# Performance work log

Measured on AMD Instinct MI355X. Metric: run time of the kernel, lower is better.

Reference implementation:

```python
import jax, jax.numpy as jnp
import numpy as np

# GE2E batch structure: N_SPK speakers, M_UTT utterances each (grouped contiguously),
# first half enrollment (-> centroid), second half test.
N_SPK, M_UTT, D = 1024, 32, 512
M_ENR = M_UTT // 2
EPS = 1e-8  # F.cosine_similarity default eps (clamps norms)


def setup_inputs() -> dict:
    key = jax.random.key(0)
    emb = jax.random.normal(key, (N_SPK * M_UTT, D), dtype=jnp.float32)
    labels = jnp.repeat(jnp.arange(N_SPK, dtype=jnp.int64), M_UTT)
    alpha = jnp.asarray(10.0, dtype=jnp.float32)
    beta = jnp.asarray(-5.0, dtype=jnp.float32)
    return {"embeddings": emb, "labels": labels, "alpha": alpha, "beta": beta}


def reference(embeddings, labels, alpha, beta):
    # labels are contiguously grouped: label i occupies rows [i*M_UTT, (i+1)*M_UTT)
    emb = embeddings.reshape(N_SPK, M_UTT, D)
    enroll = emb[:, :M_ENR]          # [N, M_enr, D]
    test = emb[:, M_ENR:]            # [N, M_tst, D]
    centroid = enroll.mean(axis=1)   # [N, D]

    cent_n = centroid / jnp.maximum(
        jnp.linalg.norm(centroid, axis=-1, keepdims=True), EPS)
    test_n = test / jnp.maximum(
        jnp.linalg.norm(test, axis=-1, keepdims=True), EPS)

    # S[i, j, t] = alpha * cos(centroid_i, test_{j,t}) + beta
    S = alpha * jnp.einsum('id,jtd->ijt', cent_n, test_n) + beta
    E = jnp.exp(S)                                   # [N, N, M_tst]

    idx = jnp.arange(N_SPK)
    pos_sum = E[idx, idx].sum(axis=-1)               # diag: own test vs own centroid
    neg_sum = E.sum(axis=(1, 2)) - pos_sum           # all other speakers' test utts

    loss = (jnp.log(neg_sum) - jnp.log(pos_sum)).mean()
    return loss
```

## Files before the change

kernel.cpp:

```cpp
#include <hip/hip_runtime.h>
#include <math.h>

#define N_SPK 1024
#define M_UTT 32
#define M_ENR 16
#define M_TEST 16
#define D 512
#define N_TEST_ROWS (N_SPK * M_TEST)


typedef __attribute__((ext_vector_type(4))) float f32x4;
typedef __attribute__((ext_vector_type(8))) short short8;
typedef __attribute__((ext_vector_type(8))) unsigned short ushort8;

typedef const __attribute__((address_space(1))) void g_void;
typedef __attribute__((address_space(3))) void lds_void;

__device__ __forceinline__ unsigned short f2bf(float f) {
    unsigned int u = __float_as_uint(f);
    u += 0x7FFF + ((u >> 16) & 1);
    return (unsigned short)(u >> 16);
}

__global__ __launch_bounds__(256) void prep_kernel(const float* __restrict__ emb,
                                                   unsigned short* __restrict__ cent,
                                                   unsigned short* __restrict__ test,
                                                   float* __restrict__ g_row,
                                                   float* __restrict__ g_pos) {
    const int b = blockIdx.x;
    const int tid = threadIdx.x;
    const int lane = tid & 63;
    const int wid = tid >> 6;

    if (b < 4) {
        g_row[b * 256 + tid] = 0.f;
        g_pos[b * 256 + tid] = 0.f;
    }

    if (b < N_SPK) {
        const float* base = emb + (size_t)b * M_UTT * D;
        float a0 = 0.f, a1 = 0.f;
#pragma unroll
        for (int u = 0; u < M_ENR; ++u) {
            a0 += base[u * D + tid];
            a1 += base[u * D + tid + 256];
        }
        a0 *= (1.f / 16.f);
        a1 *= (1.f / 16.f);
        float ss = a0 * a0 + a1 * a1;
#pragma unroll
        for (int m = 1; m < 64; m <<= 1) ss += __shfl_xor(ss, m, 64);
        __shared__ float wss[4];
        if (lane == 0) wss[wid] = ss;
        __syncthreads();
        const float tot = wss[0] + wss[1] + wss[2] + wss[3];
        const float inv = 1.f / fmaxf(sqrtf(tot), 1e-8f);
        cent[b * D + tid] = f2bf(a0 * inv);
        cent[b * D + tid + 256] = f2bf(a1 * inv);
    } else {
        const int r = (b - N_SPK) * 4 + wid;
        const int s = r >> 4, t = r & 15;
        const float* row = emb + ((size_t)s * M_UTT + M_ENR + t) * D;
        const f32x4* rv = (const f32x4*)row;
        const f32x4 v0 = rv[lane * 2];
        const f32x4 v1 = rv[lane * 2 + 1];
        float ss = v0[0]*v0[0] + v0[1]*v0[1] + v0[2]*v0[2] + v0[3]*v0[3]
                 + v1[0]*v1[0] + v1[1]*v1[1] + v1[2]*v1[2] + v1[3]*v1[3];
#pragma unroll
        for (int m = 1; m < 64; m <<= 1) ss += __shfl_xor(ss, m, 64);
        const float inv = 1.f / fmaxf(sqrtf(ss), 1e-8f);
        ushort8 o;
        o[0] = f2bf(v0[0] * inv); o[1] = f2bf(v0[1] * inv);
        o[2] = f2bf(v0[2] * inv); o[3] = f2bf(v0[3] * inv);
        o[4] = f2bf(v1[0] * inv); o[5] = f2bf(v1[1] * inv);
        o[6] = f2bf(v1[2] * inv); o[7] = f2bf(v1[3] * inv);
        *(ushort8*)&test[(size_t)r * D + lane * 8] = o;
    }
}

__global__ __launch_bounds__(512, 2) void gemm_kernel(const unsigned short* __restrict__ A,
                                                      const unsigned short* __restrict__ B,
                                                      const float* __restrict__ alpha_p,
                                                      const float* __restrict__ beta_p,
                                                      float* __restrict__ g_row,
                                                      float* __restrict__ g_pos) {
    __shared__ __align__(16) unsigned short As[128 * 512];
    __shared__ float rowsum[128];
    __shared__ float possum[128];

    const int tid = threadIdx.x;
    const int lane = tid & 63;
    const int w = tid >> 6;

    const int raw = blockIdx.x;
    const int wg = (raw & 7) * 32 + (raw >> 3);
    const int bi = wg & 7;
    const int bj = wg >> 3;
    const int row0 = bi * 128, col0 = bj * 512;
    const bool has_diag = ((bj >> 2) == bi);

#pragma unroll
    for (int it = 0; it < 16; ++it) {
        const int r = it * 8 + w;
        const int src = (row0 + r) * D + ((lane * 8) ^ ((r & 7) << 3));
        __builtin_amdgcn_global_load_lds((g_void*)&A[src],
                                         (lds_void*)&As[r * D],
                                         16, 0, 0);
    }
    if (tid < 128) { rowsum[tid] = 0.f; possum[tid] = 0.f; }

    const float alpha = *alpha_p;
    const float beta = *beta_p;

    const int bcol = col0 + w * 64;
    const unsigned short* bp[4];
#pragma unroll
    for (int ni = 0; ni < 4; ++ni)
        bp[ni] = &B[(size_t)(bcol + ni * 16 + (lane & 15)) * D + (lane >> 4) * 8];

    const int hs = ((lane >> 4) * 8) ^ ((lane & 7) << 3);
    const int arow_base = (lane & 15) * D;

    f32x4 acc[8][4] = {};
    short8 b0[4], b1[4], b2[4], b3[4];

#define LOADB(dst, kk)                                             \
    {                                                              \
        _Pragma("unroll") for (int ni = 0; ni < 4; ++ni)           \
            dst[ni] = *(const short8*)(bp[ni] + (kk));             \
    }

#define STEP(bfr, kk)                                                          \
    {                                                                          \
        const int ofs_ = (kk) ^ hs;                                            \
        _Pragma("unroll") for (int mi = 0; mi < 8; ++mi) {                     \
            const short8 af_ = *(const short8*)&As[mi * 16 * D + arow_base + ofs_]; \
            _Pragma("unroll") for (int ni = 0; ni < 4; ++ni)                   \
                acc[mi][ni] = __builtin_amdgcn_mfma_f32_16x16x32_bf16(         \
                    af_, bfr[ni], acc[mi][ni], 0, 0, 0);                       \
        }                                                                      \
    }

    LOADB(b0, 0); LOADB(b1, 32); LOADB(b2, 64); LOADB(b3, 96);
    __syncthreads();

    STEP(b0, 0);    LOADB(b0, 128);
    STEP(b1, 32);   LOADB(b1, 160);
    STEP(b2, 64);   LOADB(b2, 192);
    STEP(b3, 96);   LOADB(b3, 224);
    STEP(b0, 128);  LOADB(b0, 256);
    STEP(b1, 160);  LOADB(b1, 288);
    STEP(b2, 192);  LOADB(b2, 320);
    STEP(b3, 224);  LOADB(b3, 352);
    STEP(b0, 256);  LOADB(b0, 384);
    STEP(b1, 288);  LOADB(b1, 416);
    STEP(b2, 320);  LOADB(b2, 448);
    STEP(b3, 352);  LOADB(b3, 480);
    STEP(b0, 384);
    STEP(b1, 416);
    STEP(b2, 448);
    STEP(b3, 480);

#pragma unroll
    for (int mi = 0; mi < 8; ++mi) {
#pragma unroll
        for (int r = 0; r < 4; ++r) {
            const int lrow = mi * 16 + ((lane >> 4) << 2) + r;
            const int grow = row0 + lrow;
            float tot = 0.f, pos = 0.f;
#pragma unroll
            for (int ni = 0; ni < 4; ++ni) {
                const int gcol = bcol + ni * 16 + (lane & 15);
                const float e = __expf(fmaf(alpha, acc[mi][ni][r], beta));
                tot += e;
                if (has_diag) pos += ((gcol >> 4) == grow) ? e : 0.f;
            }
#pragma unroll
            for (int m = 1; m < 16; m <<= 1) tot += __shfl_xor(tot, m, 64);
            if (has_diag) {
#pragma unroll
                for (int m = 1; m < 16; m <<= 1) pos += __shfl_xor(pos, m, 64);
            }
            if ((lane & 15) == 0) {
                atomicAdd(&rowsum[lrow], tot);
                if (has_diag) atomicAdd(&possum[lrow], pos);
            }
        }
    }
    __syncthreads();
    if (tid < 128) {
        atomicAdd(&g_row[row0 + tid], rowsum[tid]);
        if (has_diag) atomicAdd(&g_pos[row0 + tid], possum[tid]);
    }
#undef LOADB
#undef STEP
}

__global__ __launch_bounds__(1024) void finalize_kernel(const float* __restrict__ g_row,
                                                        const float* __restrict__ g_pos,
                                                        float* __restrict__ out) {
    __shared__ float wsum[16];
    const int i = threadIdx.x;
    const int lane = i & 63, wid = i >> 6;
    const float pos = g_pos[i];
    const float neg = g_row[i] - pos;
    float v = logf(fmaxf(neg, 1e-30f)) - logf(fmaxf(pos, 1e-30f));
#pragma unroll
    for (int m = 1; m < 64; m <<= 1) v += __shfl_xor(v, m, 64);
    if (lane == 0) wsum[wid] = v;
    __syncthreads();
    if (i < 64) {
        float s = (i < 16) ? wsum[i] : 0.f;
#pragma unroll
        for (int m = 1; m < 16; m <<= 1) s += __shfl_xor(s, m, 64);
        if (i == 0) out[0] = s * (1.f / 1024.f);
    }
}

extern "C" void kernel_launch(void* const* d_in, const int* in_sizes, int n_in,
                              void* d_out, int out_size, void* d_ws, size_t ws_size,
                              hipStream_t stream) {
    const float* emb = (const float*)d_in[0];
    const float* alpha_p = (const float*)d_in[2];
    const float* beta_p = (const float*)d_in[3];

    unsigned short* cent = (unsigned short*)d_ws;
    unsigned short* test = cent + (size_t)N_SPK * D;
    float* g_row = (float*)(test + (size_t)N_TEST_ROWS * D);
    float* g_pos = g_row + N_SPK;

    prep_kernel<<<N_SPK + N_TEST_ROWS / 4, 256, 0, stream>>>(emb, cent, test, g_row, g_pos);

    gemm_kernel<<<256, 512, 0, stream>>>(cent, test, alpha_p, beta_p, g_row, g_pos);

    finalize_kernel<<<1, 1024, 0, stream>>>(g_row, g_pos, (float*)d_out);
}
```

Before: 49.81 us.

## Software-pipeline LDS A-fragment loads against MFMAs with setprio, drop occupancy hint

```diff
diff --git a/kernel.cpp b/kernel.cpp
--- a/kernel.cpp
+++ b/kernel.cpp
@@ -78,7 +78,7 @@
     }
 }
 
-__global__ __launch_bounds__(512, 2) void gemm_kernel(const unsigned short* __restrict__ A,
+__global__ __launch_bounds__(512, 1) void gemm_kernel(const unsigned short* __restrict__ A,
                                                       const unsigned short* __restrict__ B,
                                                       const float* __restrict__ alpha_p,
                                                       const float* __restrict__ beta_p,
@@ -104,8 +104,7 @@
         const int r = it * 8 + w;
         const int src = (row0 + r) * D + ((lane * 8) ^ ((r & 7) << 3));
         __builtin_amdgcn_global_load_lds((g_void*)&A[src],
-                                         (lds_void*)&As[r * D],
-                                         16, 0, 0);
+                                         (lds_void*)&As[r * D], 16, 0, 0);
     }
     if (tid < 128) { rowsum[tid] = 0.f; possum[tid] = 0.f; }
 
@@ -113,53 +112,68 @@
     const float beta = *beta_p;
 
     const int bcol = col0 + w * 64;
+    const int l15 = lane & 15;
     const unsigned short* bp[4];
 #pragma unroll
     for (int ni = 0; ni < 4; ++ni)
-        bp[ni] = &B[(size_t)(bcol + ni * 16 + (lane & 15)) * D + (lane >> 4) * 8];
+        bp[ni] = &B[(size_t)(bcol + ni * 16 + l15) * D + (lane >> 4) * 8];
 
     const int hs = ((lane >> 4) * 8) ^ ((lane & 7) << 3);
-    const int arow_base = (lane & 15) * D;
 
     f32x4 acc[8][4] = {};
-    short8 b0[4], b1[4], b2[4], b3[4];
-
-#define LOADB(dst, kk)                                             \
-    {                                                              \
-        _Pragma("unroll") for (int ni = 0; ni < 4; ++ni)           \
-            dst[ni] = *(const short8*)(bp[ni] + (kk));             \
-    }
-
-#define STEP(bfr, kk)                                                          \
+    short8 afA[4], afB[4], b0[4], b1[4];
+
+#define LOADB(dst, kk)                                              \
+    {                                                               \
+        _Pragma("unroll") for (int ni = 0; ni < 4; ++ni)            \
+            dst[ni] = *(const short8*)(bp[ni] + (kk));              \
+    }
+#define AFL(dst, kk, g)                                                        \
     {                                                                          \
         const int ofs_ = (kk) ^ hs;                                            \
-        _Pragma("unroll") for (int mi = 0; mi < 8; ++mi) {                     \
-            const short8 af_ = *(const short8*)&As[mi * 16 * D + arow_base + ofs_]; \
+        _Pragma("unroll") for (int j = 0; j < 4; ++j)                          \
+            dst[j] = *(const short8*)&As[((g) * 64 + j * 16 + l15) * D + ofs_];\
+    }
+#define PMFMA(af, bb, g)                                                       \
+    {                                                                          \
+        __builtin_amdgcn_s_setprio(1);                                         \
+        _Pragma("unroll") for (int j = 0; j < 4; ++j)                          \
             _Pragma("unroll") for (int ni = 0; ni < 4; ++ni)                   \
-                acc[mi][ni] = __builtin_amdgcn_mfma_f32_16x16x32_bf16(         \
-                    af_, bfr[ni], acc[mi][ni], 0, 0, 0);                       \
-        }                                                                      \
-    }
-
-    LOADB(b0, 0); LOADB(b1, 32); LOADB(b2, 64); LOADB(b3, 96);
+                acc[(g) * 4 + j][ni] = __builtin_amdgcn_mfma_f32_16x16x32_bf16(\
+                    af[j], bb[ni], acc[(g) * 4 + j][ni], 0, 0, 0);             \
+        __builtin_amdgcn_s_setprio(0);                                         \
+    }
+#define QSTEP(kk, bCur)                  \
+    AFL(afB, kk, 1);                     \
+    PMFMA(afA, bCur, 0);                 \
+    AFL(afA, ((kk) + 32) & 511, 0);      \
+    PMFMA(afB, bCur, 1);
+
+    LOADB(b0, 0); LOADB(b1, 32);
     __syncthreads();
-
-    STEP(b0, 0);    LOADB(b0, 128);
-    STEP(b1, 32);   LOADB(b1, 160);
-    STEP(b2, 64);   LOADB(b2, 192);
-    STEP(b3, 96);   LOADB(b3, 224);
-    STEP(b0, 128);  LOADB(b0, 256);
-    STEP(b1, 160);  LOADB(b1, 288);
-    STEP(b2, 192);  LOADB(b2, 320);
-    STEP(b3, 224);  LOADB(b3, 352);
-    STEP(b0, 256);  LOADB(b0, 384);
-    STEP(b1, 288);  LOADB(b1, 416);
-    STEP(b2, 320);  LOADB(b2, 448);
-    STEP(b3, 352);  LOADB(b3, 480);
-    STEP(b0, 384);
-    STEP(b1, 416);
-    STEP(b2, 448);
-    STEP(b3, 480);
+    AFL(afA, 0, 0);
+
+    QSTEP(0, b0);
+    LOADB(b0, 64);   QSTEP(32, b1);
+    LOADB(b1, 96);   QSTEP(64, b0);
+    LOADB(b0, 128);  QSTEP(96, b1);
+    LOADB(b1, 160);  QSTEP(128, b0);
+    LOADB(b0, 192);  QSTEP(160, b1);
+    LOADB(b1, 224);  QSTEP(192, b0);
+    LOADB(b0, 256);  QSTEP(224, b1);
+    LOADB(b1, 288);  QSTEP(256, b0);
+    LOADB(b0, 320);  QSTEP(288, b1);
+    LOADB(b1, 352);  QSTEP(320, b0);
+    LOADB(b0, 384);  QSTEP(352, b1);
+    LOADB(b1, 416);  QSTEP(384, b0);
+    LOADB(b0, 448);  QSTEP(416, b1);
+    LOADB(b1, 480);  QSTEP(448, b0);
+    QSTEP(480, b1);
+
+#undef LOADB
+#undef AFL
+#undef PMFMA
+#undef QSTEP
 
 #pragma unroll
     for (int mi = 0; mi < 8; ++mi) {
@@ -170,7 +184,7 @@
             float tot = 0.f, pos = 0.f;
 #pragma unroll
             for (int ni = 0; ni < 4; ++ni) {
-                const int gcol = bcol + ni * 16 + (lane & 15);
+                const int gcol = bcol + ni * 16 + l15;
                 const float e = __expf(fmaf(alpha, acc[mi][ni][r], beta));
                 tot += e;
                 if (has_diag) pos += ((gcol >> 4) == grow) ? e : 0.f;
@@ -181,7 +195,7 @@
 #pragma unroll
                 for (int m = 1; m < 16; m <<= 1) pos += __shfl_xor(pos, m, 64);
             }
-            if ((lane & 15) == 0) {
+            if (l15 == 0) {
                 atomicAdd(&rowsum[lrow], tot);
                 if (has_diag) atomicAdd(&possum[lrow], pos);
             }
@@ -192,8 +206,6 @@
         atomicAdd(&g_row[row0 + tid], rowsum[tid]);
         if (has_diag) atomicAdd(&g_pos[row0 + tid], possum[tid]);
     }
-#undef LOADB
-#undef STEP
 }
 
 __global__ __launch_bounds__(1024) void finalize_kernel(const float* __restrict__ g_row,
```

Result: faster. 48.58 us (-2.5%).

## Split GEMM block work across 16 waves with narrower per-wave column tiles

Applied to the files above, without the earlier changes.

```diff
diff --git a/kernel.cpp b/kernel.cpp
--- a/kernel.cpp
+++ b/kernel.cpp
@@ -78,12 +78,12 @@
     }
 }
 
-__global__ __launch_bounds__(512, 2) void gemm_kernel(const unsigned short* __restrict__ A,
-                                                      const unsigned short* __restrict__ B,
-                                                      const float* __restrict__ alpha_p,
-                                                      const float* __restrict__ beta_p,
-                                                      float* __restrict__ g_row,
-                                                      float* __restrict__ g_pos) {
+__global__ __launch_bounds__(1024) void gemm_kernel(const unsigned short* __restrict__ A,
+                                                    const unsigned short* __restrict__ B,
+                                                    const float* __restrict__ alpha_p,
+                                                    const float* __restrict__ beta_p,
+                                                    float* __restrict__ g_row,
+                                                    float* __restrict__ g_pos) {
     __shared__ __align__(16) unsigned short As[128 * 512];
     __shared__ float rowsum[128];
     __shared__ float possum[128];
@@ -91,6 +91,7 @@
     const int tid = threadIdx.x;
     const int lane = tid & 63;
     const int w = tid >> 6;
+    const int l15 = lane & 15;
 
     const int raw = blockIdx.x;
     const int wg = (raw & 7) * 32 + (raw >> 3);
@@ -100,34 +101,33 @@
     const bool has_diag = ((bj >> 2) == bi);
 
 #pragma unroll
-    for (int it = 0; it < 16; ++it) {
-        const int r = it * 8 + w;
+    for (int it = 0; it < 8; ++it) {
+        const int r = it * 16 + w;
         const int src = (row0 + r) * D + ((lane * 8) ^ ((r & 7) << 3));
         __builtin_amdgcn_global_load_lds((g_void*)&A[src],
-                                         (lds_void*)&As[r * D],
-                                         16, 0, 0);
+                                         (lds_void*)&As[r * D], 16, 0, 0);
     }
     if (tid < 128) { rowsum[tid] = 0.f; possum[tid] = 0.f; }
 
     const float alpha = *alpha_p;
     const float beta = *beta_p;
 
-    const int bcol = col0 + w * 64;
-    const unsigned short* bp[4];
-#pragma unroll
-    for (int ni = 0; ni < 4; ++ni)
-        bp[ni] = &B[(size_t)(bcol + ni * 16 + (lane & 15)) * D + (lane >> 4) * 8];
+    const int bcol = col0 + w * 32;
+    const unsigned short* bp[2];
+#pragma unroll
+    for (int ni = 0; ni < 2; ++ni)
+        bp[ni] = &B[(size_t)(bcol + ni * 16 + l15) * D + (lane >> 4) * 8];
 
     const int hs = ((lane >> 4) * 8) ^ ((lane & 7) << 3);
-    const int arow_base = (lane & 15) * D;
-
-    f32x4 acc[8][4] = {};
-    short8 b0[4], b1[4], b2[4], b3[4];
-
-#define LOADB(dst, kk)                                             \
-    {                                                              \
-        _Pragma("unroll") for (int ni = 0; ni < 4; ++ni)           \
-            dst[ni] = *(const short8*)(bp[ni] + (kk));             \
+    const int arow_base = l15 * D;
+
+    f32x4 acc[8][2] = {};
+    short8 b0[2], b1[2];
+
+#define LOADB(dst, kk)                                              \
+    {                                                               \
+        _Pragma("unroll") for (int ni = 0; ni < 2; ++ni)            \
+            dst[ni] = *(const short8*)(bp[ni] + (kk));              \
     }
 
 #define STEP(bfr, kk)                                                          \
@@ -135,31 +135,21 @@
         const int ofs_ = (kk) ^ hs;                                            \
         _Pragma("unroll") for (int mi = 0; mi < 8; ++mi) {                     \
             const short8 af_ = *(const short8*)&As[mi * 16 * D + arow_base + ofs_]; \
-            _Pragma("unroll") for (int ni = 0; ni < 4; ++ni)                   \
+            _Pragma("unroll") for (int ni = 0; ni < 2; ++ni)                   \
                 acc[mi][ni] = __builtin_amdgcn_mfma_f32_16x16x32_bf16(         \
                     af_, bfr[ni], acc[mi][ni], 0, 0, 0);                       \
         }                                                                      \
     }
 
-    LOADB(b0, 0); LOADB(b1, 32); LOADB(b2, 64); LOADB(b3, 96);
+    LOADB(b0, 0); LOADB(b1, 32);
     __syncthreads();
 
-    STEP(b0, 0);    LOADB(b0, 128);
-    STEP(b1, 32);   LOADB(b1, 160);
-    STEP(b2, 64);   LOADB(b2, 192);
-    STEP(b3, 96);   LOADB(b3, 224);
-    STEP(b0, 128);  LOADB(b0, 256);
-    STEP(b1, 160);  LOADB(b1, 288);
-    STEP(b2, 192);  LOADB(b2, 320);
-    STEP(b3, 224);  LOADB(b3, 352);
-    STEP(b0, 256);  LOADB(b0, 384);
-    STEP(b1, 288);  LOADB(b1, 416);
-    STEP(b2, 320);  LOADB(b2, 448);
-    STEP(b3, 352);  LOADB(b3, 480);
-    STEP(b0, 384);
-    STEP(b1, 416);
-    STEP(b2, 448);
-    STEP(b3, 480);
+    for (int ko = 0; ko < D; ko += 64) {
+        STEP(b0, ko);       LOADB(b0, (ko + 64) & (D - 1));
+        STEP(b1, ko + 32);  LOADB(b1, (ko + 96) & (D - 1));
+    }
+#undef LOADB
+#undef STEP
 
 #pragma unroll
     for (int mi = 0; mi < 8; ++mi) {
@@ -169,8 +159,8 @@
             const int grow = row0 + lrow;
             float tot = 0.f, pos = 0.f;
 #pragma unroll
-            for (int ni = 0; ni < 4; ++ni) {
-                const int gcol = bcol + ni * 16 + (lane & 15);
+            for (int ni = 0; ni < 2; ++ni) {
+                const int gcol = bcol + ni * 16 + l15;
                 const float e = __expf(fmaf(alpha, acc[mi][ni][r], beta));
                 tot += e;
                 if (has_diag) pos += ((gcol >> 4) == grow) ? e : 0.f;
@@ -181,7 +171,7 @@
 #pragma unroll
                 for (int m = 1; m < 16; m <<= 1) pos += __shfl_xor(pos, m, 64);
             }
-            if ((lane & 15) == 0) {
+            if (l15 == 0) {
                 atomicAdd(&rowsum[lrow], tot);
                 if (has_diag) atomicAdd(&possum[lrow], pos);
             }
@@ -192,8 +182,6 @@
         atomicAdd(&g_row[row0 + tid], rowsum[tid]);
         if (has_diag) atomicAdd(&g_pos[row0 + tid], possum[tid]);
     }
-#undef LOADB
-#undef STEP
 }
 
 __global__ __launch_bounds__(1024) void finalize_kernel(const float* __restrict__ g_row,
@@ -231,7 +219,7 @@
 
     prep_kernel<<<N_SPK + N_TEST_ROWS / 4, 256, 0, stream>>>(emb, cent, test, g_row, g_pos);
 
-    gemm_kernel<<<256, 512, 0, stream>>>(cent, test, alpha_p, beta_p, g_row, g_pos);
+    gemm_kernel<<<256, 1024, 0, stream>>>(cent, test, alpha_p, beta_p, g_row, g_pos);
 
     finalize_kernel<<<1, 1024, 0, stream>>>(g_row, g_pos, (float*)d_out);
 }
```

Result: slower. 53.18 us (+6.8%).
